# Optimization experiments

Measured on AMD Instinct MI355X. Metric: run time of the kernel, lower is better.

The kernel has to match this reference:

```python
import jax, jax.numpy as jnp
import numpy as np

NUM_USERS = 100000
NUM_ITEMS = 200000
D = 128          # embedding_dim
K = 4            # num interest heads
B = 4096
H = 256          # history length
H1, H2 = 512, 256  # hidden_units


def setup_inputs() -> dict:
    key = jax.random.key(0)
    ks = jax.random.split(key, 10)
    inp = {
        "user_ids": jax.random.randint(ks[0], (B,), 0, NUM_USERS),
        "candidate_items": jax.random.randint(ks[1], (B,), 0, NUM_ITEMS),
        "history_items": jax.random.randint(ks[2], (B, H), 0, NUM_ITEMS),
        "item_table": jax.random.normal(ks[3], (NUM_ITEMS, D), dtype=jnp.float32) * 0.05,
        "Wp": jax.random.normal(ks[4], (D, K), dtype=jnp.float32) * (1.0 / np.sqrt(D)),
        "W1": jax.random.normal(ks[5], (2 * D, H1), dtype=jnp.float32) * (1.0 / np.sqrt(2 * D)),
        "b1": jnp.zeros((H1,), dtype=jnp.float32),
        "W2": jax.random.normal(ks[6], (H1, H2), dtype=jnp.float32) * (1.0 / np.sqrt(H1)),
        "b2": jnp.zeros((H2,), dtype=jnp.float32),
        "W3": jax.random.normal(ks[7], (H2, 1), dtype=jnp.float32) * (1.0 / np.sqrt(H2)),
        "b3": jnp.zeros((1,), dtype=jnp.float32),
    }
    return inp


def reference(user_ids, candidate_items, history_items, item_table, Wp,
              W1, b1, W2, b2, W3, b3):
    # user_ids is unused by the original forward (user_emb never applied)
    item_vecs = item_table[history_items]          # (B, H, D)
    cand_vec = item_table[candidate_items]         # (B, D)

    # per-interest attention scores, softmax over history axis
    scores = jnp.einsum('bhd,dk->bhk', item_vecs, Wp)   # (B, H, K)
    scores = jax.nn.softmax(scores, axis=1)

    # softmax-weighted pooling -> K interest vectors per user
    interest_vectors = jnp.einsum('bhk,bhd->bkd', scores, item_vecs)  # (B, K, D)

    # similarity to candidate, pick best interest (data-dependent gather)
    sim_scores = jnp.einsum('bkd,bd->bk', interest_vectors, cand_vec)  # (B, K)
    best_idx = jnp.argmax(sim_scores, axis=-1)                          # (B,)
    selected = jnp.take_along_axis(
        interest_vectors, best_idx[:, None, None], axis=1)[:, 0, :]    # (B, D)

    # MLP tail: [2D -> 512] ReLU [512 -> 256] ReLU [256 -> 1], sigmoid
    x = jnp.concatenate([selected, cand_vec], axis=-1)  # (B, 2D)
    x = jax.nn.relu(x @ W1 + b1)
    x = jax.nn.relu(x @ W2 + b2)
    out = (x @ W3 + b3)[:, 0]                            # (B,)
    return jax.nn.sigmoid(out)
```

## Files before the change

### kernel.cpp

```cpp
#include <hip/hip_runtime.h>
#include <hip/hip_bf16.h>
#include <math.h>

#define B_SZ   4096
#define H_LEN  256
#define D_DIM  128
#define K_HEADS 4
#define H1_DIM 512
#define H2_DIM 256
#define NUM_ITEMS 200000

#define CH     64
#define NCH    4
#define TP2    136
#define TPAD   132

typedef __attribute__((ext_vector_type(8))) short bf16x8;
typedef __attribute__((ext_vector_type(4))) float f32x4;
typedef __attribute__((ext_vector_type(4))) float cf4;
typedef __attribute__((ext_vector_type(4))) unsigned cu4;

#define LDS_BARRIER() do {                                   \
    asm volatile("s_waitcnt lgkmcnt(0)" ::: "memory");       \
    __builtin_amdgcn_s_barrier();                            \
} while (0)

__device__ __forceinline__ float bf2f(short s) {
    unsigned u = ((unsigned)(unsigned short)s) << 16;
    float f; __builtin_memcpy(&f, &u, 4); return f;
}

__global__ __launch_bounds__(256, 4) void interest_kernel_bf16(
    const int*   __restrict__ cand_ids,
    const int*   __restrict__ hist,
    const float* __restrict__ table,
    const __hip_bfloat16* __restrict__ tableB,
    const float* __restrict__ Wp,
    __hip_bfloat16* __restrict__ Xbf)
{
    __shared__ __align__(16) short tileB[CH * TP2];
    __shared__ float wpt[K_HEADS * D_DIM];
    __shared__ float exps4[CH * 4];
    __shared__ float candv[D_DIM];
    __shared__ int   rowids[H_LEN];
    __shared__ float lsumW[16];
    __shared__ float simred[4][K_HEADS];
    __shared__ int   bestk;

    const int b    = blockIdx.x;
    const int t    = threadIdx.x;
    const int lane = t & 63, w = t >> 6;
    const int r    = t >> 2, q = t & 3;
    const int d    = t & 127, half = t >> 7;

    if (t < D_DIM) {
        float4 w4 = ((const float4*)Wp)[t];
        wpt[0 * D_DIM + t] = w4.x;
        wpt[1 * D_DIM + t] = w4.y;
        wpt[2 * D_DIM + t] = w4.z;
        wpt[3 * D_DIM + t] = w4.w;
    }
    const int cand = cand_ids[b];
    if (t >= 128 && t < 160) {
        int c = t - 128;
        ((float4*)candv)[c] = ((const float4*)(table + (long long)cand * D_DIM))[c];
    }
    rowids[t] = hist[(long long)b * H_LEN + t];

    bf16x8 v0, v1, v2, v3;
    {
        const int row0 = hist[(long long)b * H_LEN + r];
        const __hip_bfloat16* rp = tableB + (long long)row0 * D_DIM + (q << 3);
        v0 = *(const bf16x8*)(rp + 0 * 32);
        v1 = *(const bf16x8*)(rp + 1 * 32);
        v2 = *(const bf16x8*)(rp + 2 * 32);
        v3 = *(const bf16x8*)(rp + 3 * 32);
    }

    LDS_BARRIER();

    float a0 = 0.f, a1 = 0.f, a2 = 0.f, a3 = 0.f;
    float l0 = 0.f, l1 = 0.f, l2 = 0.f, l3 = 0.f;

    for (int c = 0; c < NCH; ++c) {
        bf16x8 u0, u1, u2, u3;
        if (c + 1 < NCH) {
            const int row = rowids[((c + 1) << 6) + r];
            const __hip_bfloat16* rp = tableB + (long long)row * D_DIM + (q << 3);
            u0 = *(const bf16x8*)(rp + 0 * 32);
            u1 = *(const bf16x8*)(rp + 1 * 32);
            u2 = *(const bf16x8*)(rp + 2 * 32);
            u3 = *(const bf16x8*)(rp + 3 * 32);
        }

        float s0 = 0.f, s1 = 0.f, s2 = 0.f, s3 = 0.f;
        #define DO_J(JJ, VV)                                                    \
        {   const int cb = (q << 3) + (JJ << 5);                                \
            float f0 = bf2f(VV[0]), f1 = bf2f(VV[1]);                           \
            float f2 = bf2f(VV[2]), f3 = bf2f(VV[3]);                           \
            float f4 = bf2f(VV[4]), f5 = bf2f(VV[5]);                           \
            float f6 = bf2f(VV[6]), f7 = bf2f(VV[7]);                           \
            float4 wA, wB;                                                      \
            wA = *(const float4*)(wpt + 0 * D_DIM + cb);                        \
            wB = *(const float4*)(wpt + 0 * D_DIM + cb + 4);                    \
            s0 += f0*wA.x + f1*wA.y + f2*wA.z + f3*wA.w                         \
                + f4*wB.x + f5*wB.y + f6*wB.z + f7*wB.w;                        \
            wA = *(const float4*)(wpt + 1 * D_DIM + cb);                        \
            wB = *(const float4*)(wpt + 1 * D_DIM + cb + 4);                    \
            s1 += f0*wA.x + f1*wA.y + f2*wA.z + f3*wA.w                         \
                + f4*wB.x + f5*wB.y + f6*wB.z + f7*wB.w;                        \
            wA = *(const float4*)(wpt + 2 * D_DIM + cb);                        \
            wB = *(const float4*)(wpt + 2 * D_DIM + cb + 4);                    \
            s2 += f0*wA.x + f1*wA.y + f2*wA.z + f3*wA.w                         \
                + f4*wB.x + f5*wB.y + f6*wB.z + f7*wB.w;                        \
            wA = *(const float4*)(wpt + 3 * D_DIM + cb);                        \
            wB = *(const float4*)(wpt + 3 * D_DIM + cb + 4);                    \
            s3 += f0*wA.x + f1*wA.y + f2*wA.z + f3*wA.w                         \
                + f4*wB.x + f5*wB.y + f6*wB.z + f7*wB.w;                        \
            *(bf16x8*)(tileB + r * TP2 + cb) = VV;                              \
        }
        DO_J(0, v0) DO_J(1, v1) DO_J(2, v2) DO_J(3, v3)
        #undef DO_J

        s0 += __shfl_xor(s0, 1); s0 += __shfl_xor(s0, 2);
        s1 += __shfl_xor(s1, 1); s1 += __shfl_xor(s1, 2);
        s2 += __shfl_xor(s2, 1); s2 += __shfl_xor(s2, 2);
        s3 += __shfl_xor(s3, 1); s3 += __shfl_xor(s3, 2);

        float e0 = expf(s0), e1 = expf(s1), e2 = expf(s2), e3 = expf(s3);
        if (q == 0) ((float4*)exps4)[r] = make_float4(e0, e1, e2, e3);

        float t0 = e0, t1 = e1, t2 = e2, t3 = e3;
        #pragma unroll
        for (int off = 4; off <= 32; off <<= 1) {
            t0 += __shfl_xor(t0, off);
            t1 += __shfl_xor(t1, off);
            t2 += __shfl_xor(t2, off);
            t3 += __shfl_xor(t3, off);
        }
        l0 += t0; l1 += t1; l2 += t2; l3 += t3;

        LDS_BARRIER();

        #pragma unroll 8
        for (int i = 0; i < 32; ++i) {
            int hl = (half << 5) + i;
            float4 e4 = ((const float4*)exps4)[hl];
            float  vv = bf2f(tileB[hl * TP2 + d]);
            a0 += e4.x * vv; a1 += e4.y * vv; a2 += e4.z * vv; a3 += e4.w * vv;
        }

        LDS_BARRIER();

        if (c + 1 < NCH) { v0 = u0; v1 = u1; v2 = u2; v3 = u3; }
    }

    __syncthreads();
    float* partBp = (float*)tileB;
    float* ivbufp = (float*)tileB + 512;

    if (half == 1) ((float4*)partBp)[d] = make_float4(a0, a1, a2, a3);
    if (lane == 0) ((float4*)lsumW)[w]  = make_float4(l0, l1, l2, l3);
    __syncthreads();

    float s0 = 0.f, s1 = 0.f, s2 = 0.f, s3 = 0.f;
    if (half == 0) {
        float4 pb = ((const float4*)partBp)[d];
        float4 L0 = ((const float4*)lsumW)[0];
        float4 L1 = ((const float4*)lsumW)[1];
        float4 L2 = ((const float4*)lsumW)[2];
        float4 L3 = ((const float4*)lsumW)[3];
        float i0 = 1.f / (L0.x + L1.x + L2.x + L3.x);
        float i1 = 1.f / (L0.y + L1.y + L2.y + L3.y);
        float i2 = 1.f / (L0.z + L1.z + L2.z + L3.z);
        float i3 = 1.f / (L0.w + L1.w + L2.w + L3.w);
        a0 = (a0 + pb.x) * i0;
        a1 = (a1 + pb.y) * i1;
        a2 = (a2 + pb.z) * i2;
        a3 = (a3 + pb.w) * i3;
        ((float4*)ivbufp)[d] = make_float4(a0, a1, a2, a3);
        float cd = candv[d];
        s0 = a0 * cd; s1 = a1 * cd; s2 = a2 * cd; s3 = a3 * cd;
    }
    #pragma unroll
    for (int off = 32; off >= 1; off >>= 1) {
        s0 += __shfl_xor(s0, off);
        s1 += __shfl_xor(s1, off);
        s2 += __shfl_xor(s2, off);
        s3 += __shfl_xor(s3, off);
    }
    if (lane == 0) {
        simred[w][0] = s0; simred[w][1] = s1;
        simred[w][2] = s2; simred[w][3] = s3;
    }
    __syncthreads();

    if (t == 0) {
        float sim[4];
        #pragma unroll
        for (int k = 0; k < 4; ++k)
            sim[k] = simred[0][k] + simred[1][k] + simred[2][k] + simred[3][k];
        int best = 0;
        #pragma unroll
        for (int k = 1; k < 4; ++k) if (sim[k] > sim[best]) best = k;
        bestk = best;
    }
    __syncthreads();

    __hip_bfloat16* xrow = Xbf + (long long)b * (2 * D_DIM);
    if (t < 128) xrow[t] = __float2bfloat16(ivbufp[t * 4 + bestk]);
    else         xrow[t] = __float2bfloat16(candv[t - 128]);
}

__global__ __launch_bounds__(256, 6) void interest_kernel_f32(
    const int*   __restrict__ cand_ids, const int* __restrict__ hist,
    const float* __restrict__ table, const float* __restrict__ Wp,
    __hip_bfloat16* __restrict__ Xbf)
{
    __shared__ float tile[32 * TPAD];
    __shared__ float wpt[K_HEADS * D_DIM];
    __shared__ float exps4[32 * 4];
    __shared__ float candv[D_DIM];
    __shared__ int   rowids[H_LEN];
    __shared__ float lsumW[16];
    __shared__ float simred[4][K_HEADS];
    __shared__ int   bestk;

    const int b    = blockIdx.x;
    const int t    = threadIdx.x;
    const int lane = t & 63, w = t >> 6;
    const int r    = t >> 3, q = t & 7;
    const int d    = t & 127, half = t >> 7;

    if (t < D_DIM) {
        float4 w4 = ((const float4*)Wp)[t];
        wpt[0 * D_DIM + t] = w4.x; wpt[1 * D_DIM + t] = w4.y;
        wpt[2 * D_DIM + t] = w4.z; wpt[3 * D_DIM + t] = w4.w;
    }
    const int cand = cand_ids[b];
    if (t >= 128 && t < 160) {
        int c = t - 128;
        ((float4*)candv)[c] = ((const float4*)(table + (long long)cand * D_DIM))[c];
    }
    rowids[t] = hist[(long long)b * H_LEN + t];

    float4 v0, v1, v2, v3;
    {
        const int row0 = hist[(long long)b * H_LEN + r];
        const float* rp = table + (long long)row0 * D_DIM + (q << 2);
        v0 = *(const float4*)(rp + 0 * 32); v1 = *(const float4*)(rp + 1 * 32);
        v2 = *(const float4*)(rp + 2 * 32); v3 = *(const float4*)(rp + 3 * 32);
    }
    LDS_BARRIER();

    float a0 = 0.f, a1 = 0.f, a2 = 0.f, a3 = 0.f;
    float l0 = 0.f, l1 = 0.f, l2 = 0.f, l3 = 0.f;

    for (int c = 0; c < 8; ++c) {
        float4 u0, u1, u2, u3;
        if (c + 1 < 8) {
            const int row = rowids[((c + 1) << 5) + r];
            const float* rp = table + (long long)row * D_DIM + (q << 2);
            u0 = *(const float4*)(rp + 0 * 32); u1 = *(const float4*)(rp + 1 * 32);
            u2 = *(const float4*)(rp + 2 * 32); u3 = *(const float4*)(rp + 3 * 32);
        }
        float s0 = 0.f, s1 = 0.f, s2 = 0.f, s3 = 0.f;
        float4 va;
        #define DO_J(JJ, VV)                                                    \
        {   va = VV;                                                            \
            const int cb = (q << 2) + (JJ << 5);                                \
            float4 w0 = *(const float4*)(wpt + 0 * D_DIM + cb);                 \
            float4 w1 = *(const float4*)(wpt + 1 * D_DIM + cb);                 \
            float4 w2 = *(const float4*)(wpt + 2 * D_DIM + cb);                 \
            float4 w3 = *(const float4*)(wpt + 3 * D_DIM + cb);                 \
            s0 += va.x*w0.x + va.y*w0.y + va.z*w0.z + va.w*w0.w;                \
            s1 += va.x*w1.x + va.y*w1.y + va.z*w1.z + va.w*w1.w;                \
            s2 += va.x*w2.x + va.y*w2.y + va.z*w2.z + va.w*w2.w;                \
            s3 += va.x*w3.x + va.y*w3.y + va.z*w3.z + va.w*w3.w;                \
            *(float4*)(tile + r * TPAD + cb) = va;                              \
        }
        DO_J(0, v0) DO_J(1, v1) DO_J(2, v2) DO_J(3, v3)
        #undef DO_J

        s0 += __shfl_xor(s0, 1); s0 += __shfl_xor(s0, 2); s0 += __shfl_xor(s0, 4);
        s1 += __shfl_xor(s1, 1); s1 += __shfl_xor(s1, 2); s1 += __shfl_xor(s1, 4);
        s2 += __shfl_xor(s2, 1); s2 += __shfl_xor(s2, 2); s2 += __shfl_xor(s2, 4);
        s3 += __shfl_xor(s3, 1); s3 += __shfl_xor(s3, 2); s3 += __shfl_xor(s3, 4);

        float e0 = expf(s0), e1 = expf(s1), e2 = expf(s2), e3 = expf(s3);
        if (q == 0) ((float4*)exps4)[r] = make_float4(e0, e1, e2, e3);

        float t0 = e0, t1 = e1, t2 = e2, t3 = e3;
        #pragma unroll
        for (int off = 8; off <= 32; off <<= 1) {
            t0 += __shfl_xor(t0, off); t1 += __shfl_xor(t1, off);
            t2 += __shfl_xor(t2, off); t3 += __shfl_xor(t3, off);
        }
        l0 += t0; l1 += t1; l2 += t2; l3 += t3;

        LDS_BARRIER();
        #pragma unroll
        for (int i = 0; i < 16; ++i) {
            int hl = (half << 4) + i;
            float4 e4 = ((const float4*)exps4)[hl];
            float  vv = tile[hl * TPAD + d];
            a0 += e4.x * vv; a1 += e4.y * vv; a2 += e4.z * vv; a3 += e4.w * vv;
        }
        LDS_BARRIER();
        if (c + 1 < 8) { v0 = u0; v1 = u1; v2 = u2; v3 = u3; }
    }

    __syncthreads();
    float* partBp = tile;
    float* ivbufp = tile + 512;

    if (half == 1) ((float4*)partBp)[d] = make_float4(a0, a1, a2, a3);
    if (lane == 0) ((float4*)lsumW)[w]  = make_float4(l0, l1, l2, l3);
    __syncthreads();

    float s0 = 0.f, s1 = 0.f, s2 = 0.f, s3 = 0.f;
    if (half == 0) {
        float4 pb = ((const float4*)partBp)[d];
        float4 L0 = ((const float4*)lsumW)[0];
        float4 L1 = ((const float4*)lsumW)[1];
        float4 L2 = ((const float4*)lsumW)[2];
        float4 L3 = ((const float4*)lsumW)[3];
        float i0 = 1.f / (L0.x + L1.x + L2.x + L3.x);
        float i1 = 1.f / (L0.y + L1.y + L2.y + L3.y);
        float i2 = 1.f / (L0.z + L1.z + L2.z + L3.z);
        float i3 = 1.f / (L0.w + L1.w + L2.w + L3.w);
        a0 = (a0 + pb.x) * i0; a1 = (a1 + pb.y) * i1;
        a2 = (a2 + pb.z) * i2; a3 = (a3 + pb.w) * i3;
        ((float4*)ivbufp)[d] = make_float4(a0, a1, a2, a3);
        float cd = candv[d];
        s0 = a0 * cd; s1 = a1 * cd; s2 = a2 * cd; s3 = a3 * cd;
    }
    #pragma unroll
    for (int off = 32; off >= 1; off >>= 1) {
        s0 += __shfl_xor(s0, off); s1 += __shfl_xor(s1, off);
        s2 += __shfl_xor(s2, off); s3 += __shfl_xor(s3, off);
    }
    if (lane == 0) {
        simred[w][0] = s0; simred[w][1] = s1;
        simred[w][2] = s2; simred[w][3] = s3;
    }
    __syncthreads();
    if (t == 0) {
        float sim[4];
        #pragma unroll
        for (int k = 0; k < 4; ++k)
            sim[k] = simred[0][k] + simred[1][k] + simred[2][k] + simred[3][k];
        int best = 0;
        #pragma unroll
        for (int k = 1; k < 4; ++k) if (sim[k] > sim[best]) best = k;
        bestk = best;
    }
    __syncthreads();

    __hip_bfloat16* xrow = Xbf + (long long)b * (2 * D_DIM);
    if (t < 128) xrow[t] = __float2bfloat16(ivbufp[t * 4 + bestk]);
    else         xrow[t] = __float2bfloat16(candv[t - 128]);
}

__global__ __launch_bounds__(256) void convert_all(
    const float* __restrict__ table,
    const float* __restrict__ W1, const float* __restrict__ W2,
    __hip_bfloat16* __restrict__ tableB,
    __hip_bfloat16* __restrict__ W1t, __hip_bfloat16* __restrict__ W2t)
{
    __shared__ float tl[32][33];
    int bid = blockIdx.x;
    if (bid < 6250) {
        long long idx = (long long)bid * 256 + threadIdx.x;
        const cf4* s = (const cf4*)table + idx * 4;
        #pragma unroll
        for (int hh = 0; hh < 2; ++hh) {
            cf4 s0 = __builtin_nontemporal_load(s + hh * 2 + 0);
            cf4 s1 = __builtin_nontemporal_load(s + hh * 2 + 1);
            __hip_bfloat16 o[8];
            o[0] = __float2bfloat16(s0.x); o[1] = __float2bfloat16(s0.y);
            o[2] = __float2bfloat16(s0.z); o[3] = __float2bfloat16(s0.w);
            o[4] = __float2bfloat16(s1.x); o[5] = __float2bfloat16(s1.y);
            o[6] = __float2bfloat16(s1.z); o[7] = __float2bfloat16(s1.w);
            cu4 ov; __builtin_memcpy(&ov, o, 16);
            __builtin_nontemporal_store(ov, (cu4*)(tableB + idx * 16 + hh * 8));
        }
        return;
    }
    bid -= 6250;
    const float* W; __hip_bfloat16* Wt; int K, N;
    if (bid < 128) { W = W1; Wt = W1t; K = 2 * D_DIM; N = H1_DIM; }
    else           { W = W2; Wt = W2t; K = H1_DIM;    N = H2_DIM; bid -= 128; }
    const int ntn = N >> 5;
    const int k0 = (bid / ntn) << 5, n0 = (bid % ntn) << 5;
    const int tx = threadIdx.x & 31, ty = threadIdx.x >> 5;
    #pragma unroll
    for (int j = 0; j < 4; ++j)
        tl[ty + 8 * j][tx] = W[(long long)(k0 + ty + 8 * j) * N + n0 + tx];
    __syncthreads();
    #pragma unroll
    for (int j = 0; j < 4; ++j)
        Wt[(long long)(n0 + ty + 8 * j) * K + k0 + tx] =
            __float2bfloat16(tl[tx][ty + 8 * j]);
}

__global__ __launch_bounds__(256) void convert_weights(
    const float* __restrict__ W1, const float* __restrict__ W2,
    __hip_bfloat16* __restrict__ W1t, __hip_bfloat16* __restrict__ W2t)
{
    __shared__ float tl[32][33];
    int bid = blockIdx.x;
    const float* W; __hip_bfloat16* Wt; int K, N;
    if (bid < 128) { W = W1; Wt = W1t; K = 2 * D_DIM; N = H1_DIM; }
    else           { W = W2; Wt = W2t; K = H1_DIM;    N = H2_DIM; bid -= 128; }
    const int ntn = N >> 5;
    const int k0 = (bid / ntn) << 5, n0 = (bid % ntn) << 5;
    const int tx = threadIdx.x & 31, ty = threadIdx.x >> 5;
    #pragma unroll
    for (int j = 0; j < 4; ++j)
        tl[ty + 8 * j][tx] = W[(long long)(k0 + ty + 8 * j) * N + n0 + tx];
    __syncthreads();
    #pragma unroll
    for (int j = 0; j < 4; ++j)
        Wt[(long long)(n0 + ty + 8 * j) * K + k0 + tx] =
            __float2bfloat16(tl[tx][ty + 8 * j]);
}

__global__ __launch_bounds__(512) void mlp_fused(
    const __hip_bfloat16* __restrict__ X,
    const __hip_bfloat16* __restrict__ W1t,
    const float* __restrict__ b1,
    const __hip_bfloat16* __restrict__ W2t,
    const float* __restrict__ b2,
    const float* __restrict__ W3,
    const float* __restrict__ b3,
    float*       __restrict__ out)
{
    __shared__ __hip_bfloat16 h1[16][H1_DIM + 8];
    __shared__ float          h2[16][H2_DIM + 4];

    const int t    = threadIdx.x;
    const int wave = t >> 6, lane = t & 63;
    const int lm   = lane & 15, quad = lane >> 4;
    const int m0   = blockIdx.x * 16;

    const __hip_bfloat16* Ap = X + (long long)(m0 + lm) * (2 * D_DIM) + quad * 8;
    bf16x8 af[8];
    #pragma unroll
    for (int it = 0; it < 8; ++it) af[it] = *(const bf16x8*)(Ap + it * 32);

    #pragma unroll
    for (int tn = 0; tn < 4; ++tn) {
        const int n0 = (wave * 4 + tn) * 16;
        const __hip_bfloat16* Bp = W1t + (long long)(n0 + lm) * (2 * D_DIM) + quad * 8;
        f32x4 acc = {0.f, 0.f, 0.f, 0.f};
        #pragma unroll
        for (int it = 0; it < 8; ++it) {
            bf16x8 bfr = *(const bf16x8*)(Bp + it * 32);
            acc = __builtin_amdgcn_mfma_f32_16x16x32_bf16(af[it], bfr, acc, 0, 0, 0);
        }
        const float bv = b1[n0 + lm];
        #pragma unroll
        for (int i = 0; i < 4; ++i)
            h1[quad * 4 + i][n0 + lm] = __float2bfloat16(fmaxf(acc[i] + bv, 0.f));
    }
    __syncthreads();

    bf16x8 a2[16];
    #pragma unroll
    for (int it = 0; it < 16; ++it)
        a2[it] = *(const bf16x8*)(&h1[lm][quad * 8 + it * 32]);

    #pragma unroll
    for (int tn = 0; tn < 2; ++tn) {
        const int n0 = (wave * 2 + tn) * 16;
        const __hip_bfloat16* Bp = W2t + (long long)(n0 + lm) * H1_DIM + quad * 8;
        f32x4 acc = {0.f, 0.f, 0.f, 0.f};
        #pragma unroll
        for (int it = 0; it < 16; ++it) {
            bf16x8 bfr = *(const bf16x8*)(Bp + it * 32);
            acc = __builtin_amdgcn_mfma_f32_16x16x32_bf16(a2[it], bfr, acc, 0, 0, 0);
        }
        const float bv = b2[n0 + lm];
        #pragma unroll
        for (int i = 0; i < 4; ++i)
            h2[quad * 4 + i][n0 + lm] = fmaxf(acc[i] + bv, 0.f);
    }
    __syncthreads();

    {
        const int row = t >> 5, c = (t & 31) * 8;
        float s = 0.f;
        #pragma unroll
        for (int j = 0; j < 8; ++j) s += h2[row][c + j] * W3[c + j];
        #pragma unroll
        for (int off = 1; off <= 16; off <<= 1) s += __shfl_xor(s, off);
        if ((lane & 31) == 0)
            out[m0 + row] = 1.f / (1.f + expf(-(s + b3[0])));
    }
}

extern "C" void kernel_launch(void* const* d_in, const int* in_sizes, int n_in,
                              void* d_out, int out_size, void* d_ws, size_t ws_size,
                              hipStream_t stream) {
    const int*   cand  = (const int*)  d_in[1];
    const int*   hist  = (const int*)  d_in[2];
    const float* table = (const float*)d_in[3];
    const float* Wp    = (const float*)d_in[4];
    const float* W1    = (const float*)d_in[5];
    const float* b1    = (const float*)d_in[6];
    const float* W2    = (const float*)d_in[7];
    const float* b2    = (const float*)d_in[8];
    const float* W3    = (const float*)d_in[9];
    const float* b3    = (const float*)d_in[10];
    float* out = (float*)d_out;

    char* p = (char*)d_ws;
    __hip_bfloat16* Xbf = (__hip_bfloat16*)p;  p += (size_t)B_SZ * 2 * D_DIM * 2;
    __hip_bfloat16* W1t = (__hip_bfloat16*)p;  p += (size_t)H1_DIM * 2 * D_DIM * 2;
    __hip_bfloat16* W2t = (__hip_bfloat16*)p;  p += (size_t)H1_DIM * H2_DIM * 2;
    __hip_bfloat16* tableB = (__hip_bfloat16*)p;
    const size_t need = ((char*)tableB - (char*)d_ws) + (size_t)NUM_ITEMS * D_DIM * 2;

    if (ws_size >= need) {
        convert_all<<<6250 + 256, 256, 0, stream>>>(table, W1, W2, tableB, W1t, W2t);
        interest_kernel_bf16<<<B_SZ, 256, 0, stream>>>(cand, hist, table, tableB, Wp, Xbf);
    } else {
        convert_weights<<<256, 256, 0, stream>>>(W1, W2, W1t, W2t);
        interest_kernel_f32<<<B_SZ, 256, 0, stream>>>(cand, hist, table, Wp, Xbf);
    }
    mlp_fused<<<B_SZ / 16, 512, 0, stream>>>(Xbf, W1t, b1, W2t, b2, W3, b3, out);
}
```

Before: 282.0 us.

## Precompute per-item attention exps in convert pass and DMA history tiles to LDS

The convert pass now computes exp(item·Wp) for every item in the table into an Etab array while it writes the bf16 copy. The interest kernel then just gathers those four values per history row instead of computing the scores per batch row. History tiles are loaded straight into double-buffered LDS with global_load_lds, and vmcnt waits replace the register prefetch. This removes the repeated score math and register staging, at the cost of projecting all 200k items every call and no max-subtraction in the softmax.

Result: faster. 252.8 us (-10.4%).

```diff
diff --git a/kernel.cpp b/kernel.cpp
--- a/kernel.cpp
+++ b/kernel.cpp
@@ -12,155 +12,114 @@
 
 #define CH     64
 #define NCH    4
-#define TP2    136
 #define TPAD   132
 
 typedef __attribute__((ext_vector_type(8))) short bf16x8;
 typedef __attribute__((ext_vector_type(4))) float f32x4;
-typedef __attribute__((ext_vector_type(4))) float cf4;
-typedef __attribute__((ext_vector_type(4))) unsigned cu4;
 
 #define LDS_BARRIER() do {                                   \
     asm volatile("s_waitcnt lgkmcnt(0)" ::: "memory");       \
     __builtin_amdgcn_s_barrier();                            \
 } while (0)
 
+#define WAITVM4() asm volatile("s_waitcnt vmcnt(4)" ::: "memory")
+#define WAITVM0() asm volatile("s_waitcnt vmcnt(0)" ::: "memory")
+
 __device__ __forceinline__ float bf2f(short s) {
     unsigned u = ((unsigned)(unsigned short)s) << 16;
     float f; __builtin_memcpy(&f, &u, 4); return f;
 }
 
-__global__ __launch_bounds__(256, 4) void interest_kernel_bf16(
+__device__ __forceinline__ void gl_lds16(const void* g, void* l) {
+    __builtin_amdgcn_global_load_lds(
+        (const __attribute__((address_space(1))) void*)g,
+        (__attribute__((address_space(3))) void*)l, 16, 0, 0);
+}
+
+__global__ __launch_bounds__(256, 4) void interest_dma(
     const int*   __restrict__ cand_ids,
     const int*   __restrict__ hist,
     const float* __restrict__ table,
     const __hip_bfloat16* __restrict__ tableB,
-    const float* __restrict__ Wp,
+    const float* __restrict__ Etab,
     __hip_bfloat16* __restrict__ Xbf)
 {
-    __shared__ __align__(16) short tileB[CH * TP2];
-    __shared__ float wpt[K_HEADS * D_DIM];
-    __shared__ float exps4[CH * 4];
+    __shared__ __align__(16) short tile2[2][CH][D_DIM];
+    __shared__ float exps[H_LEN][4];
     __shared__ float candv[D_DIM];
     __shared__ int   rowids[H_LEN];
     __shared__ float lsumW[16];
-    __shared__ float simred[4][K_HEADS];
     __shared__ int   bestk;
 
     const int b    = blockIdx.x;
     const int t    = threadIdx.x;
     const int lane = t & 63, w = t >> 6;
-    const int r    = t >> 2, q = t & 3;
     const int d    = t & 127, half = t >> 7;
 
-    if (t < D_DIM) {
-        float4 w4 = ((const float4*)Wp)[t];
-        wpt[0 * D_DIM + t] = w4.x;
-        wpt[1 * D_DIM + t] = w4.y;
-        wpt[2 * D_DIM + t] = w4.z;
-        wpt[3 * D_DIM + t] = w4.w;
-    }
     const int cand = cand_ids[b];
-    if (t >= 128 && t < 160) {
-        int c = t - 128;
-        ((float4*)candv)[c] = ((const float4*)(table + (long long)cand * D_DIM))[c];
-    }
+    if (t < 32)
+        ((float4*)candv)[t] = ((const float4*)(table + (long long)cand * D_DIM))[t];
     rowids[t] = hist[(long long)b * H_LEN + t];
-
-    bf16x8 v0, v1, v2, v3;
-    {
-        const int row0 = hist[(long long)b * H_LEN + r];
-        const __hip_bfloat16* rp = tableB + (long long)row0 * D_DIM + (q << 3);
-        v0 = *(const bf16x8*)(rp + 0 * 32);
-        v1 = *(const bf16x8*)(rp + 1 * 32);
-        v2 = *(const bf16x8*)(rp + 2 * 32);
-        v3 = *(const bf16x8*)(rp + 3 * 32);
-    }
-
-    LDS_BARRIER();
+    __syncthreads();
+
+    float4 ev = ((const float4*)Etab)[rowids[t]];
+
+    #pragma unroll
+    for (int cc = 0; cc < 2; ++cc) {
+        #pragma unroll
+        for (int i = 0; i < 4; ++i) {
+            const int rloc = w * 16 + i * 4 + (lane >> 4);
+            const int grow = rowids[(cc << 6) + rloc];
+            const __hip_bfloat16* gp =
+                tableB + (long long)grow * D_DIM + ((lane & 15) << 3);
+            gl_lds16(gp, &tile2[cc][w * 16 + i * 4][0]);
+        }
+    }
+
+    ((float4*)exps)[t] = ev;
+    float l0 = ev.x, l1 = ev.y, l2 = ev.z, l3 = ev.w;
+    #pragma unroll
+    for (int off = 1; off <= 32; off <<= 1) {
+        l0 += __shfl_xor(l0, off);
+        l1 += __shfl_xor(l1, off);
+        l2 += __shfl_xor(l2, off);
+        l3 += __shfl_xor(l3, off);
+    }
+    if (lane == 0) ((float4*)lsumW)[w] = make_float4(l0, l1, l2, l3);
 
     float a0 = 0.f, a1 = 0.f, a2 = 0.f, a3 = 0.f;
-    float l0 = 0.f, l1 = 0.f, l2 = 0.f, l3 = 0.f;
 
     for (int c = 0; c < NCH; ++c) {
-        bf16x8 u0, u1, u2, u3;
-        if (c + 1 < NCH) {
-            const int row = rowids[((c + 1) << 6) + r];
-            const __hip_bfloat16* rp = tableB + (long long)row * D_DIM + (q << 3);
-            u0 = *(const bf16x8*)(rp + 0 * 32);
-            u1 = *(const bf16x8*)(rp + 1 * 32);
-            u2 = *(const bf16x8*)(rp + 2 * 32);
-            u3 = *(const bf16x8*)(rp + 3 * 32);
-        }
-
-        float s0 = 0.f, s1 = 0.f, s2 = 0.f, s3 = 0.f;
-        #define DO_J(JJ, VV)                                                    \
-        {   const int cb = (q << 3) + (JJ << 5);                                \
-            float f0 = bf2f(VV[0]), f1 = bf2f(VV[1]);                           \
-            float f2 = bf2f(VV[2]), f3 = bf2f(VV[3]);                           \
-            float f4 = bf2f(VV[4]), f5 = bf2f(VV[5]);                           \
-            float f6 = bf2f(VV[6]), f7 = bf2f(VV[7]);                           \
-            float4 wA, wB;                                                      \
-            wA = *(const float4*)(wpt + 0 * D_DIM + cb);                        \
-            wB = *(const float4*)(wpt + 0 * D_DIM + cb + 4);                    \
-            s0 += f0*wA.x + f1*wA.y + f2*wA.z + f3*wA.w                         \
-                + f4*wB.x + f5*wB.y + f6*wB.z + f7*wB.w;                        \
-            wA = *(const float4*)(wpt + 1 * D_DIM + cb);                        \
-            wB = *(const float4*)(wpt + 1 * D_DIM + cb + 4);                    \
-            s1 += f0*wA.x + f1*wA.y + f2*wA.z + f3*wA.w                         \
-                + f4*wB.x + f5*wB.y + f6*wB.z + f7*wB.w;                        \
-            wA = *(const float4*)(wpt + 2 * D_DIM + cb);                        \
-            wB = *(const float4*)(wpt + 2 * D_DIM + cb + 4);                    \
-            s2 += f0*wA.x + f1*wA.y + f2*wA.z + f3*wA.w                         \
-                + f4*wB.x + f5*wB.y + f6*wB.z + f7*wB.w;                        \
-            wA = *(const float4*)(wpt + 3 * D_DIM + cb);                        \
-            wB = *(const float4*)(wpt + 3 * D_DIM + cb + 4);                    \
-            s3 += f0*wA.x + f1*wA.y + f2*wA.z + f3*wA.w                         \
-                + f4*wB.x + f5*wB.y + f6*wB.z + f7*wB.w;                        \
-            *(bf16x8*)(tileB + r * TP2 + cb) = VV;                              \
-        }
-        DO_J(0, v0) DO_J(1, v1) DO_J(2, v2) DO_J(3, v3)
-        #undef DO_J
-
-        s0 += __shfl_xor(s0, 1); s0 += __shfl_xor(s0, 2);
-        s1 += __shfl_xor(s1, 1); s1 += __shfl_xor(s1, 2);
-        s2 += __shfl_xor(s2, 1); s2 += __shfl_xor(s2, 2);
-        s3 += __shfl_xor(s3, 1); s3 += __shfl_xor(s3, 2);
-
-        float e0 = expf(s0), e1 = expf(s1), e2 = expf(s2), e3 = expf(s3);
-        if (q == 0) ((float4*)exps4)[r] = make_float4(e0, e1, e2, e3);
-
-        float t0 = e0, t1 = e1, t2 = e2, t3 = e3;
-        #pragma unroll
-        for (int off = 4; off <= 32; off <<= 1) {
-            t0 += __shfl_xor(t0, off);
-            t1 += __shfl_xor(t1, off);
-            t2 += __shfl_xor(t2, off);
-            t3 += __shfl_xor(t3, off);
-        }
-        l0 += t0; l1 += t1; l2 += t2; l3 += t3;
-
+        if (c < NCH - 1) WAITVM4(); else WAITVM0();
         LDS_BARRIER();
 
         #pragma unroll 8
         for (int i = 0; i < 32; ++i) {
-            int hl = (half << 5) + i;
-            float4 e4 = ((const float4*)exps4)[hl];
-            float  vv = bf2f(tileB[hl * TP2 + d]);
+            const int hl = (half << 5) + i;
+            float4 e4 = ((const float4*)exps)[(c << 6) + hl];
+            float  vv = bf2f(tile2[c & 1][hl][d]);
             a0 += e4.x * vv; a1 += e4.y * vv; a2 += e4.z * vv; a3 += e4.w * vv;
         }
 
         LDS_BARRIER();
 
-        if (c + 1 < NCH) { v0 = u0; v1 = u1; v2 = u2; v3 = u3; }
-    }
-
-    __syncthreads();
-    float* partBp = (float*)tileB;
-    float* ivbufp = (float*)tileB + 512;
+        if (c + 2 < NCH) {
+            #pragma unroll
+            for (int i = 0; i < 4; ++i) {
+                const int rloc = w * 16 + i * 4 + (lane >> 4);
+                const int grow = rowids[((c + 2) << 6) + rloc];
+                const __hip_bfloat16* gp =
+                    tableB + (long long)grow * D_DIM + ((lane & 15) << 3);
+                gl_lds16(gp, &tile2[c & 1][w * 16 + i * 4][0]);
+            }
+        }
+    }
+
+    __syncthreads();
+    float* partBp = (float*)tile2;
+    float* ivbufp = (float*)tile2 + 512;
 
     if (half == 1) ((float4*)partBp)[d] = make_float4(a0, a1, a2, a3);
-    if (lane == 0) ((float4*)lsumW)[w]  = make_float4(l0, l1, l2, l3);
     __syncthreads();
 
     float s0 = 0.f, s1 = 0.f, s2 = 0.f, s3 = 0.f;
@@ -189,6 +148,7 @@
         s2 += __shfl_xor(s2, off);
         s3 += __shfl_xor(s3, off);
     }
+    __shared__ float simred[4][K_HEADS];
     if (lane == 0) {
         simred[w][0] = s0; simred[w][1] = s1;
         simred[w][2] = s2; simred[w][3] = s3;
@@ -363,28 +323,53 @@
 }
 
 __global__ __launch_bounds__(256) void convert_all(
-    const float* __restrict__ table,
+    const float* __restrict__ table, const float* __restrict__ Wp,
     const float* __restrict__ W1, const float* __restrict__ W2,
-    __hip_bfloat16* __restrict__ tableB,
+    __hip_bfloat16* __restrict__ tableB, float* __restrict__ Etab,
     __hip_bfloat16* __restrict__ W1t, __hip_bfloat16* __restrict__ W2t)
 {
     __shared__ float tl[32][33];
+    __shared__ float wpt[K_HEADS][D_DIM];
     int bid = blockIdx.x;
+    const int tid = threadIdx.x;
     if (bid < 6250) {
-        long long idx = (long long)bid * 256 + threadIdx.x;
-        const cf4* s = (const cf4*)table + idx * 4;
-        #pragma unroll
-        for (int hh = 0; hh < 2; ++hh) {
-            cf4 s0 = __builtin_nontemporal_load(s + hh * 2 + 0);
-            cf4 s1 = __builtin_nontemporal_load(s + hh * 2 + 1);
-            __hip_bfloat16 o[8];
-            o[0] = __float2bfloat16(s0.x); o[1] = __float2bfloat16(s0.y);
-            o[2] = __float2bfloat16(s0.z); o[3] = __float2bfloat16(s0.w);
-            o[4] = __float2bfloat16(s1.x); o[5] = __float2bfloat16(s1.y);
-            o[6] = __float2bfloat16(s1.z); o[7] = __float2bfloat16(s1.w);
-            cu4 ov; __builtin_memcpy(&ov, o, 16);
-            __builtin_nontemporal_store(ov, (cu4*)(tableB + idx * 16 + hh * 8));
-        }
+        if (tid < D_DIM) {
+            float4 w4 = ((const float4*)Wp)[tid];
+            wpt[0][tid] = w4.x; wpt[1][tid] = w4.y;
+            wpt[2][tid] = w4.z; wpt[3][tid] = w4.w;
+        }
+        __syncthreads();
+        const int r = tid >> 3, q = tid & 7;
+        const long long row = (long long)bid * 32 + r;
+        const float* src = table + row * D_DIM + q * 16;
+        float x[16];
+        #pragma unroll
+        for (int j = 0; j < 4; ++j) {
+            float4 v = ((const float4*)src)[j];
+            x[4*j] = v.x; x[4*j+1] = v.y; x[4*j+2] = v.z; x[4*j+3] = v.w;
+        }
+        __hip_bfloat16 o[16];
+        #pragma unroll
+        for (int j = 0; j < 16; ++j) o[j] = __float2bfloat16(x[j]);
+        __hip_bfloat16* dst = tableB + row * D_DIM + q * 16;
+        ((uint4*)dst)[0] = *(uint4*)(o);
+        ((uint4*)dst)[1] = *(uint4*)(o + 8);
+
+        float s0 = 0.f, s1 = 0.f, s2 = 0.f, s3 = 0.f;
+        const int cb = q * 16;
+        #pragma unroll
+        for (int j = 0; j < 16; ++j) {
+            s0 += x[j] * wpt[0][cb + j];
+            s1 += x[j] * wpt[1][cb + j];
+            s2 += x[j] * wpt[2][cb + j];
+            s3 += x[j] * wpt[3][cb + j];
+        }
+        s0 += __shfl_xor(s0, 1); s0 += __shfl_xor(s0, 2); s0 += __shfl_xor(s0, 4);
+        s1 += __shfl_xor(s1, 1); s1 += __shfl_xor(s1, 2); s1 += __shfl_xor(s1, 4);
+        s2 += __shfl_xor(s2, 1); s2 += __shfl_xor(s2, 2); s2 += __shfl_xor(s2, 4);
+        s3 += __shfl_xor(s3, 1); s3 += __shfl_xor(s3, 2); s3 += __shfl_xor(s3, 4);
+        if (q == 0)
+            ((float4*)Etab)[row] = make_float4(expf(s0), expf(s1), expf(s2), expf(s3));
         return;
     }
     bid -= 6250;
@@ -393,7 +378,7 @@
     else           { W = W2; Wt = W2t; K = H1_DIM;    N = H2_DIM; bid -= 128; }
     const int ntn = N >> 5;
     const int k0 = (bid / ntn) << 5, n0 = (bid % ntn) << 5;
-    const int tx = threadIdx.x & 31, ty = threadIdx.x >> 5;
+    const int tx = tid & 31, ty = tid >> 5;
     #pragma unroll
     for (int j = 0; j < 4; ++j)
         tl[ty + 8 * j][tx] = W[(long long)(k0 + ty + 8 * j) * N + n0 + tx];
@@ -519,12 +504,14 @@
     __hip_bfloat16* Xbf = (__hip_bfloat16*)p;  p += (size_t)B_SZ * 2 * D_DIM * 2;
     __hip_bfloat16* W1t = (__hip_bfloat16*)p;  p += (size_t)H1_DIM * 2 * D_DIM * 2;
     __hip_bfloat16* W2t = (__hip_bfloat16*)p;  p += (size_t)H1_DIM * H2_DIM * 2;
-    __hip_bfloat16* tableB = (__hip_bfloat16*)p;
-    const size_t need = ((char*)tableB - (char*)d_ws) + (size_t)NUM_ITEMS * D_DIM * 2;
+    __hip_bfloat16* tableB = (__hip_bfloat16*)p; p += (size_t)NUM_ITEMS * D_DIM * 2;
+    float*          Etab   = (float*)p;
+    const size_t need = ((char*)Etab - (char*)d_ws) + (size_t)NUM_ITEMS * 4 * 4;
 
     if (ws_size >= need) {
-        convert_all<<<6250 + 256, 256, 0, stream>>>(table, W1, W2, tableB, W1t, W2t);
-        interest_kernel_bf16<<<B_SZ, 256, 0, stream>>>(cand, hist, table, tableB, Wp, Xbf);
+        convert_all<<<6250 + 256, 256, 0, stream>>>(table, Wp, W1, W2,
+                                                    tableB, Etab, W1t, W2t);
+        interest_dma<<<B_SZ, 256, 0, stream>>>(cand, hist, table, tableB, Etab, Xbf);
     } else {
         convert_weights<<<256, 256, 0, stream>>>(W1, W2, W1t, W2t);
         interest_kernel_f32<<<B_SZ, 256, 0, stream>>>(cand, hist, table, Wp, Xbf);
```
